# Performance work log

Hardware: AMD Instinct MI355X
Metric: run time of the kernel (lower is better)

Reference implementation:

```python
import jax, jax.numpy as jnp
import numpy as np

NUM_ITERS = 5
TEMP = 0.1


def setup_inputs() -> dict:
    key = jax.random.key(0)
    k1, k2 = jax.random.split(key)
    pred_masks = jax.random.uniform(k1, (1, 100, 512, 512), dtype=jnp.float32)
    gt_masks = jax.random.uniform(k2, (50, 512, 512), dtype=jnp.float32)
    return {"pred_masks": pred_masks, "gt_masks": gt_masks}


def reference(pred_masks, gt_masks):
    # pred_masks: [B=1, K, H, W]; gt_masks: [N, H, W]
    gt = gt_masks[None]  # [1, N, H, W]
    # cost[b,k,n] = 1 - <pred_k, gt_n> over HW
    cost = 1.0 - jnp.einsum('bkhw,bnhw->bkn', pred_masks, gt)
    log_alpha = -cost / TEMP  # [1, K, N]
    for _ in range(NUM_ITERS):
        log_alpha = log_alpha - jax.nn.logsumexp(log_alpha, axis=2, keepdims=True)
        log_alpha = log_alpha - jax.nn.logsumexp(log_alpha, axis=1, keepdims=True)
    return jnp.exp(log_alpha)
```

## Files before the change

### kernel.cpp

```cpp
#include <hip/hip_runtime.h>
#include <math.h>

#define HW       262144
#define TOTSTEPS (HW / 32)
#define MROWS    100
#define NCOLS    50
#define OUTSZ    (MROWS * NCOLS)

typedef __attribute__((ext_vector_type(8))) _Float16 f16x8;
typedef __attribute__((ext_vector_type(2))) __fp16   fp16x2;
typedef __attribute__((ext_vector_type(4))) float    f32x4;

#define ABYTES   12800
#define BUFBYTES 20480

typedef __attribute__((address_space(1))) const unsigned int GU32;
typedef __attribute__((address_space(3))) unsigned int LU32;

__device__ __forceinline__ void split_f16(const float4& v0, const float4& v1,
                                          f16x8& hi, f16x8& lo) {
  float xs[8] = {v0.x, v0.y, v0.z, v0.w, v1.x, v1.y, v1.z, v1.w};
  union { fp16x2 p[4]; f16x8 v; } H, L;
#pragma unroll
  for (int j = 0; j < 4; ++j) {
    H.p[j] = __builtin_amdgcn_cvt_pkrtz(xs[2 * j], xs[2 * j + 1]);
    float l0 = xs[2 * j]     - (float)H.p[j][0];
    float l1 = xs[2 * j + 1] - (float)H.p[j][1];
    L.p[j] = __builtin_amdgcn_cvt_pkrtz(l0, l1);
  }
  hi = H.v; lo = L.v;
}

__global__ __launch_bounds__(256, 2) void dm_phase1(
    const float* __restrict__ pred, const float* __restrict__ gt,
    float* __restrict__ partial, int nblk) {
  __shared__ unsigned char smem[3 * BUFBYTES];

  const int b    = blockIdx.x;
  const int tid  = threadIdx.x;
  const int lane = tid & 63;
  const int wid  = tid >> 6;
  const int wi = wid >> 1, wj = wid & 1;
  const int g = lane >> 4, r = lane & 15;

  const int k0s = (int)(((long)b * TOTSTEPS) / nblk);
  const int k1s = (int)(((long)(b + 1) * TOTSTEPS) / nblk);
  const int nst = k1s - k0s;

  const float* srcb[5];
#pragma unroll
  for (int it = 0; it < 5; ++it) {
    int s = it * 256 + tid;
    const float* p;
    if (s < 800) {
      int row = s >> 3, t = s & 7;
      p = pred + (size_t)row * HW + ((t ^ (row & 7)) << 2);
    } else if (s < 1200) {
      int s2 = s - 800;
      int row = s2 >> 3, t = s2 & 7;
      p = gt + (size_t)row * HW + ((t ^ (row & 7)) << 2);
    } else {
      p = pred + ((s - 1200) << 2);
    }
    srcb[it] = p;
  }

  auto STAGE = [&](unsigned char* bufb, int kf) {
#pragma unroll
    for (int it = 0; it < 5; ++it)
      __builtin_amdgcn_global_load_lds((GU32*)(srcb[it] + kf),
          (LU32*)(bufb + (it * 256 + wid * 64) * 16), 16, 0, 0);
  };

  f32x4 acc[4][2] = {};

  auto COMPUTE = [&](const unsigned char* bufb) {
    f16x8 bh[2], bl[2];
#pragma unroll
    for (int nf = 0; nf < 2; ++nf) {
      int R = wj * 32 + nf * 16 + r;
      if (R > NCOLS - 1) R = NCOLS - 1;
      const unsigned char* rowb = bufb + ABYTES + R * 128;
      float4 v0 = *(const float4*)(rowb + (((2 * g    ) ^ (R & 7)) << 4));
      float4 v1 = *(const float4*)(rowb + (((2 * g + 1) ^ (R & 7)) << 4));
      split_f16(v0, v1, bh[nf], bl[nf]);
    }
#pragma unroll
    for (int mf = 0; mf < 4; ++mf) {
      if (wi == 0 || mf < 3) {
        int R = wi * 64 + mf * 16 + r;
        if (R > MROWS - 1) R = MROWS - 1;
        const unsigned char* rowb = bufb + R * 128;
        float4 v0 = *(const float4*)(rowb + (((2 * g    ) ^ (R & 7)) << 4));
        float4 v1 = *(const float4*)(rowb + (((2 * g + 1) ^ (R & 7)) << 4));
        f16x8 ah, al;
        split_f16(v0, v1, ah, al);
#pragma unroll
        for (int nf = 0; nf < 2; ++nf) {
          acc[mf][nf] = __builtin_amdgcn_mfma_f32_16x16x32_f16(ah, bh[nf], acc[mf][nf], 0, 0, 0);
          acc[mf][nf] = __builtin_amdgcn_mfma_f32_16x16x32_f16(al, bh[nf], acc[mf][nf], 0, 0, 0);
          acc[mf][nf] = __builtin_amdgcn_mfma_f32_16x16x32_f16(ah, bl[nf], acc[mf][nf], 0, 0, 0);
        }
      }
    }
  };

  STAGE(smem, k0s << 5);
  if (nst > 1) STAGE(smem + BUFBYTES, (k0s + 1) << 5);

  int qc = 0;
  for (int s = 0; s < nst; ++s) {
    if (s + 1 < nst) asm volatile("s_waitcnt vmcnt(5)" ::: "memory");
    else             asm volatile("s_waitcnt vmcnt(0)" ::: "memory");
    __builtin_amdgcn_s_barrier();
    COMPUTE(smem + qc * BUFBYTES);
    if (s + 2 < nst) {
      int qs = qc + 2; if (qs >= 3) qs -= 3;
      STAGE(smem + qs * BUFBYTES, (k0s + s + 2) << 5);
    }
    qc = (qc == 2) ? 0 : qc + 1;
  }

#pragma unroll
  for (int mf = 0; mf < 4; ++mf) {
#pragma unroll
    for (int nf = 0; nf < 2; ++nf) {
#pragma unroll
      for (int qq = 0; qq < 4; ++qq) {
        int row = wi * 64 + mf * 16 + g * 4 + qq;
        int col = wj * 32 + nf * 16 + r;
        if (row < MROWS && col < NCOLS)
          partial[(size_t)b * OUTSZ + row * NCOLS + col] = acc[mf][nf][qq];
      }
    }
  }
}

template <int NB>
__global__ void dm_reduce(const float* __restrict__ partial,
                          double* __restrict__ la0) {
  const int tid = threadIdx.x, wid = tid >> 6, lane = tid & 63;
  const int pbase = blockIdx.x * 16 + wid * 4;
  if (pbase >= OUTSZ) return;
  constexpr int IT = NB / 64;
  float4 v[IT];
#pragma unroll
  for (int i = 0; i < IT; ++i)
    v[i] = *(const float4*)(partial + (size_t)(lane + 64 * i) * OUTSZ + pbase);
  double d0 = 0, d1 = 0, d2 = 0, d3 = 0;
#pragma unroll
  for (int i = 0; i < IT; ++i) {
    d0 += (double)v[i].x; d1 += (double)v[i].y;
    d2 += (double)v[i].z; d3 += (double)v[i].w;
  }
#pragma unroll
  for (int off = 32; off; off >>= 1) {
    d0 += __shfl_xor(d0, off);
    d1 += __shfl_xor(d1, off);
    d2 += __shfl_xor(d2, off);
    d3 += __shfl_xor(d3, off);
  }
  if (lane == 0) {
    la0[pbase + 0] = (d0 - 1.0) * 10.0;
    la0[pbase + 1] = (d1 - 1.0) * 10.0;
    la0[pbase + 2] = (d2 - 1.0) * 10.0;
    la0[pbase + 3] = (d3 - 1.0) * 10.0;
  }
}

__global__ __launch_bounds__(256) void dm_sinkhorn(const double* __restrict__ la_in,
                                                   float* __restrict__ out) {
  __shared__ double la[OUTSZ];
  __shared__ double rp[MROWS];
  __shared__ double cp[NCOLS];
  const int t = threadIdx.x;
  for (int p = t; p < OUTSZ; p += 256) la[p] = la_in[p];
  if (t < NCOLS) cp[t] = 0.0;
  __syncthreads();
  for (int it = 0; it < 5; ++it) {
    if (t < 2 * MROWS) {
      int row = t >> 1, sl = t & 1;
      double m = -1e300;
      for (int j = sl; j < NCOLS; j += 2) m = fmax(m, la[row * NCOLS + j] - cp[j]);
      float s = 0.f;
      for (int j = sl; j < NCOLS; j += 2)
        s += __expf((float)(la[row * NCOLS + j] - cp[j] - m));
      double mo = __shfl_xor(m, 1); float so = __shfl_xor(s, 1);
      double mn = fmax(m, mo);
      s = s * __expf((float)(m - mn)) + so * __expf((float)(mo - mn));
      if (sl == 0) rp[row] = mn + (double)__logf(s);
    }
    __syncthreads();
    if (t < 4 * NCOLS) {
      int col = t >> 2, sl = t & 3;
      double m = -1e300;
      for (int i = sl; i < MROWS; i += 4) m = fmax(m, la[i * NCOLS + col] - rp[i]);
      float s = 0.f;
      for (int i = sl; i < MROWS; i += 4)
        s += __expf((float)(la[i * NCOLS + col] - rp[i] - m));
#pragma unroll
      for (int off = 1; off < 4; off <<= 1) {
        double mo = __shfl_xor(m, off); float so = __shfl_xor(s, off);
        double mn = fmax(m, mo);
        s = s * __expf((float)(m - mn)) + so * __expf((float)(mo - mn));
        m = mn;
      }
      if (sl == 0) cp[col] = m + (double)__logf(s);
    }
    __syncthreads();
  }
  for (int p = t; p < OUTSZ; p += 256)
    out[p] = __expf((float)(la[p] - rp[p / NCOLS] - cp[p % NCOLS]));
}

extern "C" void kernel_launch(void* const* d_in, const int* in_sizes, int n_in,
                              void* d_out, int out_size, void* d_ws, size_t ws_size,
                              hipStream_t stream) {
  const float* pred = (const float*)d_in[0];
  const float* gt   = (const float*)d_in[1];
  float* out = (float*)d_out;

  auto fits = [&](int nb) {
    return ((size_t)nb * OUTSZ * sizeof(float) + OUTSZ * sizeof(double)) <= ws_size;
  };
  int nblk = fits(512) ? 512 : 256;

  float*  partial = (float*)d_ws;
  double* la0 = (double*)((char*)d_ws + (size_t)nblk * OUTSZ * sizeof(float));

  dm_phase1<<<nblk, 256, 0, stream>>>(pred, gt, partial, nblk);
  if (nblk == 512) dm_reduce<512><<<(OUTSZ + 15) / 16, 256, 0, stream>>>(partial, la0);
  else             dm_reduce<256><<<(OUTSZ + 15) / 16, 256, 0, stream>>>(partial, la0);
  dm_sinkhorn<<<1, 256, 0, stream>>>(la0, out);
}
```

Measured before the change: 76.18 us.

## Split each block into two independent wave-pairs with private double buffers

Each 256-thread block now runs two independent 128-thread pairs, each working on its own K-chunk with a private double-buffered LDS region. Each wave computes 4 column fragments instead of 2, so the B split is not duplicated across waves. The K dimension is split into up to 1024 partial slices and the reduction kernel sums more partials. This raises per-wave MFMA work and makes the two pairs within a block overlap loads and compute independently. In exchange it adds an extra barrier per step, uses more LDS per block, and writes more partial-sum traffic.

Result: slower. 84.35 us (+10.7%).

```diff
diff --git a/kernel.cpp b/kernel.cpp
--- a/kernel.cpp
+++ b/kernel.cpp
@@ -2,7 +2,6 @@
 #include <math.h>
 
 #define HW       262144
-#define TOTSTEPS (HW / 32)
 #define MROWS    100
 #define NCOLS    50
 #define OUTSZ    (MROWS * NCOLS)
@@ -11,8 +10,8 @@
 typedef __attribute__((ext_vector_type(2))) __fp16   fp16x2;
 typedef __attribute__((ext_vector_type(4))) float    f32x4;
 
+#define PBUF     20480
 #define ABYTES   12800
-#define BUFBYTES 20480
 
 typedef __attribute__((address_space(1))) const unsigned int GU32;
 typedef __attribute__((address_space(3))) unsigned int LU32;
@@ -33,52 +32,54 @@
 
 __global__ __launch_bounds__(256, 2) void dm_phase1(
     const float* __restrict__ pred, const float* __restrict__ gt,
-    float* __restrict__ partial, int nblk) {
-  __shared__ unsigned char smem[3 * BUFBYTES];
+    float* __restrict__ partial, int npairs) {
+  __shared__ unsigned char smem[4 * PBUF];
 
   const int b    = blockIdx.x;
   const int tid  = threadIdx.x;
   const int lane = tid & 63;
   const int wid  = tid >> 6;
-  const int wi = wid >> 1, wj = wid & 1;
+  const int p    = wid >> 1;
+  const int wv   = wid & 1;
+  const int tp   = tid & 127;
   const int g = lane >> 4, r = lane & 15;
 
-  const int k0s = (int)(((long)b * TOTSTEPS) / nblk);
-  const int k1s = (int)(((long)(b + 1) * TOTSTEPS) / nblk);
-  const int nst = k1s - k0s;
-
-  const float* srcb[5];
-#pragma unroll
-  for (int it = 0; it < 5; ++it) {
-    int s = it * 256 + tid;
-    const float* p;
-    if (s < 800) {
-      int row = s >> 3, t = s & 7;
-      p = pred + (size_t)row * HW + ((t ^ (row & 7)) << 2);
-    } else if (s < 1200) {
-      int s2 = s - 800;
-      int row = s2 >> 3, t = s2 & 7;
-      p = gt + (size_t)row * HW + ((t ^ (row & 7)) << 2);
-    } else {
-      p = pred + ((s - 1200) << 2);
-    }
-    srcb[it] = p;
-  }
-
-  auto STAGE = [&](unsigned char* bufb, int kf) {
-#pragma unroll
-    for (int it = 0; it < 5; ++it)
-      __builtin_amdgcn_global_load_lds((GU32*)(srcb[it] + kf),
-          (LU32*)(bufb + (it * 256 + wid * 64) * 16), 16, 0, 0);
+  const int chunkf = HW / npairs;
+  const int nst    = chunkf >> 5;
+  const int c      = p ? (npairs - 1 - b) : b;
+  const int kbase  = c * chunkf;
+
+  const float* srcp[10];
+#pragma unroll
+  for (int it = 0; it < 10; ++it) {
+    int s = it * 128 + tp;
+    int row = s >> 3, t = s & 7;
+    const float* base;
+    int rr;
+    if (row < MROWS)      { rr = row;          base = pred; }
+    else if (row < 150)   { rr = row - MROWS;  base = gt;   }
+    else                  { rr = NCOLS - 1;    base = gt;   }
+    srcp[it] = base + (size_t)rr * HW + kbase + ((t ^ (rr & 7)) << 2);
+  }
+
+  unsigned char* pb = smem + p * 2 * PBUF;
+
+  auto STAGE = [&](int q, int s) {
+    unsigned char* bufb = pb + q * PBUF;
+#pragma unroll
+    for (int it = 0; it < 10; ++it)
+      __builtin_amdgcn_global_load_lds((GU32*)(srcp[it] + (s << 5)),
+          (LU32*)(bufb + (it * 128 + wv * 64) * 16), 16, 0, 0);
   };
 
-  f32x4 acc[4][2] = {};
-
-  auto COMPUTE = [&](const unsigned char* bufb) {
-    f16x8 bh[2], bl[2];
-#pragma unroll
-    for (int nf = 0; nf < 2; ++nf) {
-      int R = wj * 32 + nf * 16 + r;
+  f32x4 acc[4][4] = {};
+
+  auto COMPUTE = [&](int q) {
+    const unsigned char* bufb = pb + q * PBUF;
+    f16x8 bh[4], bl[4];
+#pragma unroll
+    for (int nf = 0; nf < 4; ++nf) {
+      int R = nf * 16 + r;
       if (R > NCOLS - 1) R = NCOLS - 1;
       const unsigned char* rowb = bufb + ABYTES + R * 128;
       float4 v0 = *(const float4*)(rowb + (((2 * g    ) ^ (R & 7)) << 4));
@@ -87,8 +88,8 @@
     }
 #pragma unroll
     for (int mf = 0; mf < 4; ++mf) {
-      if (wi == 0 || mf < 3) {
-        int R = wi * 64 + mf * 16 + r;
+      if (wv == 0 || mf < 3) {
+        int R = wv * 64 + mf * 16 + r;
         if (R > MROWS - 1) R = MROWS - 1;
         const unsigned char* rowb = bufb + R * 128;
         float4 v0 = *(const float4*)(rowb + (((2 * g    ) ^ (R & 7)) << 4));
@@ -96,7 +97,7 @@
         f16x8 ah, al;
         split_f16(v0, v1, ah, al);
 #pragma unroll
-        for (int nf = 0; nf < 2; ++nf) {
+        for (int nf = 0; nf < 4; ++nf) {
           acc[mf][nf] = __builtin_amdgcn_mfma_f32_16x16x32_f16(ah, bh[nf], acc[mf][nf], 0, 0, 0);
           acc[mf][nf] = __builtin_amdgcn_mfma_f32_16x16x32_f16(al, bh[nf], acc[mf][nf], 0, 0, 0);
           acc[mf][nf] = __builtin_amdgcn_mfma_f32_16x16x32_f16(ah, bl[nf], acc[mf][nf], 0, 0, 0);
@@ -105,32 +106,28 @@
     }
   };
 
-  STAGE(smem, k0s << 5);
-  if (nst > 1) STAGE(smem + BUFBYTES, (k0s + 1) << 5);
-
-  int qc = 0;
+  STAGE(0, 0);
+  if (nst > 1) STAGE(1, 1);
   for (int s = 0; s < nst; ++s) {
-    if (s + 1 < nst) asm volatile("s_waitcnt vmcnt(5)" ::: "memory");
-    else             asm volatile("s_waitcnt vmcnt(0)" ::: "memory");
+    if (s + 1 < nst) asm volatile("s_waitcnt vmcnt(10)" ::: "memory");
+    else             asm volatile("s_waitcnt vmcnt(0)"  ::: "memory");
     __builtin_amdgcn_s_barrier();
-    COMPUTE(smem + qc * BUFBYTES);
-    if (s + 2 < nst) {
-      int qs = qc + 2; if (qs >= 3) qs -= 3;
-      STAGE(smem + qs * BUFBYTES, (k0s + s + 2) << 5);
-    }
-    qc = (qc == 2) ? 0 : qc + 1;
-  }
-
+    COMPUTE(s & 1);
+    __builtin_amdgcn_s_barrier();
+    if (s + 2 < nst) STAGE(s & 1, s + 2);
+  }
+
+  const size_t obase = (size_t)(b * 2 + p) * OUTSZ;
 #pragma unroll
   for (int mf = 0; mf < 4; ++mf) {
 #pragma unroll
-    for (int nf = 0; nf < 2; ++nf) {
+    for (int nf = 0; nf < 4; ++nf) {
 #pragma unroll
       for (int qq = 0; qq < 4; ++qq) {
-        int row = wi * 64 + mf * 16 + g * 4 + qq;
-        int col = wj * 32 + nf * 16 + r;
+        int row = wv * 64 + mf * 16 + g * 4 + qq;
+        int col = nf * 16 + r;
         if (row < MROWS && col < NCOLS)
-          partial[(size_t)b * OUTSZ + row * NCOLS + col] = acc[mf][nf][qq];
+          partial[obase + row * NCOLS + col] = acc[mf][nf][qq];
       }
     }
   }
@@ -220,16 +217,17 @@
   const float* gt   = (const float*)d_in[1];
   float* out = (float*)d_out;
 
-  auto fits = [&](int nb) {
-    return ((size_t)nb * OUTSZ * sizeof(float) + OUTSZ * sizeof(double)) <= ws_size;
+  auto fits = [&](int np) {
+    return ((size_t)np * OUTSZ * sizeof(float) + OUTSZ * sizeof(double)) <= ws_size;
   };
-  int nblk = fits(512) ? 512 : 256;
+  int npairs = fits(1024) ? 1024 : (fits(512) ? 512 : 256);
 
   float*  partial = (float*)d_ws;
-  double* la0 = (double*)((char*)d_ws + (size_t)nblk * OUTSZ * sizeof(float));
-
-  dm_phase1<<<nblk, 256, 0, stream>>>(pred, gt, partial, nblk);
-  if (nblk == 512) dm_reduce<512><<<(OUTSZ + 15) / 16, 256, 0, stream>>>(partial, la0);
-  else             dm_reduce<256><<<(OUTSZ + 15) / 16, 256, 0, stream>>>(partial, la0);
+  double* la0 = (double*)((char*)d_ws + (size_t)npairs * OUTSZ * sizeof(float));
+
+  dm_phase1<<<npairs / 2, 256, 0, stream>>>(pred, gt, partial, npairs);
+  if (npairs == 1024)     dm_reduce<1024><<<(OUTSZ + 15) / 16, 256, 0, stream>>>(partial, la0);
+  else if (npairs == 512) dm_reduce<512><<<(OUTSZ + 15) / 16, 256, 0, stream>>>(partial, la0);
+  else                    dm_reduce<256><<<(OUTSZ + 15) / 16, 256, 0, stream>>>(partial, la0);
   dm_sinkhorn<<<1, 256, 0, stream>>>(la0, out);
 }
```
